# Kernel tuning notes

Hardware: AMD Instinct MI355X
Metric: run time of the kernel (lower is better)

## Reference

```python
import jax, jax.numpy as jnp
import numpy as np

T, HID, H, KV, D = 2048, 2048, 16, 8, 128
EPS = 1e-6
THETA = 10000.0


def setup_inputs() -> dict:
    key = jax.random.key(0)
    ks = jax.random.split(key, 4)
    return {
        "positions": jnp.arange(T, dtype=jnp.int32),
        "hidden_states": jax.random.normal(ks[0], (T, HID), dtype=jnp.float32),
        "layernorm_weight": jnp.ones((HID,), dtype=jnp.float32),
        "qkv_weight": jax.random.normal(ks[1], ((H + 2 * KV) * D, HID), dtype=jnp.float32) * 0.02,
        "q_norm_weight": jnp.ones((D,), dtype=jnp.float32),
        "k_norm_weight": jnp.ones((D,), dtype=jnp.float32),
        "o_weight": jax.random.normal(ks[2], (HID, H * D), dtype=jnp.float32) * 0.02,
    }


def _rms(x, w, eps=EPS):
    var = jnp.mean(jnp.square(x), axis=-1, keepdims=True)
    return x * jax.lax.rsqrt(var + eps) * w


def _rope(x, pos):
    # NeoX-style rotary over full head_dim. x: [T, nH, D]
    inv_freq = 1.0 / (THETA ** (jnp.arange(0, D, 2, dtype=jnp.float32) / D))
    ang = pos.astype(jnp.float32)[:, None] * inv_freq  # [T, D/2]
    cos, sin = jnp.cos(ang)[:, None, :], jnp.sin(ang)[:, None, :]
    x1, x2 = x[..., : D // 2], x[..., D // 2 :]
    return jnp.concatenate([x1 * cos - x2 * sin, x2 * cos + x1 * sin], axis=-1)


def reference(positions, hidden_states, layernorm_weight, qkv_weight,
              q_norm_weight, k_norm_weight, o_weight):
    # Fused RMSNorm + QKV projection
    normed = _rms(hidden_states, layernorm_weight)                 # [T, HID]
    qkv = normed @ qkv_weight.T                                    # [T, (H+2KV)*D]
    q, k, v = jnp.split(qkv, [H * D, (H + KV) * D], axis=-1)
    q = _rms(q.reshape(T, H, D), q_norm_weight)                    # per-head q norm
    k = _rms(k.reshape(T, KV, D), k_norm_weight)                   # per-head k norm
    v = v.reshape(T, KV, D)
    # RoPE
    q = _rope(q, positions)
    k = _rope(k, positions)
    # GQA causal attention
    scale = D ** -0.5
    kr = jnp.repeat(k, H // KV, axis=1)                            # [T, H, D]
    vr = jnp.repeat(v, H // KV, axis=1)
    scores = jnp.einsum("qhd,khd->hqk", q, kr) * scale             # [H, T, T]
    mask = jnp.tril(jnp.ones((T, T), dtype=bool))
    scores = jnp.where(mask[None], scores, jnp.finfo(scores.dtype).min)
    attn = jax.nn.softmax(scores, axis=-1)
    out = jnp.einsum("hqk,khd->qhd", attn, vr).reshape(T, H * D)
    return out @ o_weight.T                                        # [T, HID]
```

## Files before the change

### kernel.cpp

```cpp
#include <hip/hip_runtime.h>
#include <cstdint>
#include <cstddef>

typedef __bf16 bf16;
typedef __attribute__((ext_vector_type(8))) __bf16 bf16x8;
typedef __attribute__((ext_vector_type(4))) __bf16 bf16x4v;
typedef __attribute__((ext_vector_type(4))) float f32x4;
typedef __attribute__((ext_vector_type(4))) short short4v;

#define T_N   2048
#define HID_N 2048
#define NH    16
#define NKV   8
#define HD    128

#define MFMA(a, b, c) __builtin_amdgcn_mfma_f32_16x16x32_bf16((a), (b), (c), 0, 0, 0)

__device__ __forceinline__ f32x4 MFMA16(short4v a, short4v b, f32x4 c) {
#if __has_builtin(__builtin_amdgcn_mfma_f32_16x16x16bf16_1k)
    return __builtin_amdgcn_mfma_f32_16x16x16bf16_1k(a, b, c, 0, 0, 0);
#else
    asm volatile("v_mfma_f32_16x16x16_bf16 %0, %1, %2, %0\n\ts_nop 7\n\ts_nop 7"
                 : "+v"(c) : "v"(a), "v"(b));
    return c;
#endif
}

__device__ __forceinline__ void gl_lds16(const void* g, void* l) {
    __builtin_amdgcn_global_load_lds(
        (const __attribute__((address_space(1))) unsigned int*)g,
        (__attribute__((address_space(3))) unsigned int*)l,
        16, 0, 0);
}

__device__ __forceinline__ uint32_t pk2(float a, float b) {
    union { bf16 h; unsigned short u; } ca, cb;
    ca.h = (bf16)a; cb.h = (bf16)b;
    return ((uint32_t)cb.u << 16) | ca.u;
}

__device__ __forceinline__ void y2cq(int y, int& ci, int& qt) {
    if (y < 25)       { ci = 0; qt = y + 7; }
    else if (y < 42)  { ci = 1; qt = y - 10; }
    else if (y < 51)  { ci = 2; qt = y - 19; }
    else if (y == 51) { ci = 3; qt = 31; }
    else { int z = y - 52; int k = 7 - (z >> 2); ci = z & 3; qt = 8 * ci + k - 1; }
}
__device__ __forceinline__ int yof(int ci, int qt) {
    int k = qt + 1 - 8 * ci;
    if (k >= 8) {
        if (ci == 0) return qt - 7;
        if (ci == 1) return qt + 10;
        if (ci == 2) return qt + 19;
        return 51;
    }
    return 52 + (7 - k) * 4 + ci;
}

__global__ __launch_bounds__(256) void k_f2b(const float* __restrict__ in,
                                             bf16* __restrict__ out, int n) {
    int i = (blockIdx.x * 256 + threadIdx.x) * 8;
    if (i >= n) return;
    const float4* p = (const float4*)(in + i);
    float4 a = p[0], b = p[1];
    bf16x8 v;
    v[0] = (bf16)a.x; v[1] = (bf16)a.y; v[2] = (bf16)a.z; v[3] = (bf16)a.w;
    v[4] = (bf16)b.x; v[5] = (bf16)b.y; v[6] = (bf16)b.z; v[7] = (bf16)b.w;
    *(bf16x8*)(out + i) = v;
}

__global__ __launch_bounds__(256) void k_rmsnorm(const float* __restrict__ x,
                                                 const float* __restrict__ w,
                                                 bf16* __restrict__ out) {
    int row = blockIdx.x, tid = threadIdx.x;
    const float* xr = x + (size_t)row * HID_N;
    float4 a = ((const float4*)xr)[tid * 2];
    float4 b = ((const float4*)xr)[tid * 2 + 1];
    float ss = a.x*a.x + a.y*a.y + a.z*a.z + a.w*a.w
             + b.x*b.x + b.y*b.y + b.z*b.z + b.w*b.w;
    #pragma unroll
    for (int m = 32; m; m >>= 1) ss += __shfl_xor(ss, m);
    __shared__ float red[4];
    if ((tid & 63) == 0) red[tid >> 6] = ss;
    __syncthreads();
    float tot = red[0] + red[1] + red[2] + red[3];
    float rs = rsqrtf(tot * (1.0f / HID_N) + 1e-6f);
    const float4* wr = (const float4*)(w + tid * 8);
    float4 wa = wr[0], wb = wr[1];
    bf16x8 v;
    v[0] = (bf16)(a.x * rs * wa.x); v[1] = (bf16)(a.y * rs * wa.y);
    v[2] = (bf16)(a.z * rs * wa.z); v[3] = (bf16)(a.w * rs * wa.w);
    v[4] = (bf16)(b.x * rs * wb.x); v[5] = (bf16)(b.y * rs * wb.y);
    v[6] = (bf16)(b.z * rs * wb.z); v[7] = (bf16)(b.w * rs * wb.w);
    *(bf16x8*)(out + (size_t)row * HID_N + tid * 8) = v;
}

__global__ __launch_bounds__(256, 3) void k_gemm_bt(const bf16* __restrict__ A,
                                                    const bf16* __restrict__ B,
                                                    float* __restrict__ C,
                                                    int M, int N, int K) {
    __shared__ __attribute__((aligned(16))) bf16 As[128 * 64];
    __shared__ __attribute__((aligned(16))) bf16 Bs[128 * 64];
    const int tid = threadIdx.x;
    const int lane = tid & 63, wid = tid >> 6;
    const int wm = wid >> 1, wn = wid & 1;
    const int r = lane & 15, g = lane >> 4;
    const size_t bm = (size_t)blockIdx.y * 128, bn = (size_t)blockIdx.x * 128;

    f32x4 acc[4][4] = {};

    const int srow = tid >> 3;
    const int schk = tid & 7;

    for (int k0 = 0; k0 < K; k0 += 64) {
        __syncthreads();
        #pragma unroll
        for (int c = 0; c < 4; c++) {
            int row = c * 32 + srow;
            int ka = (schk ^ (row & 7)) << 3;
            gl_lds16(A + (bm + row) * (size_t)K + k0 + ka,
                     (char*)As + c * 4096 + tid * 16);
            gl_lds16(B + (bn + row) * (size_t)K + k0 + ka,
                     (char*)Bs + c * 4096 + tid * 16);
        }
        __syncthreads();
        #pragma unroll
        for (int kk = 0; kk < 2; kk++) {
            bf16x8 af[4], bfr[4];
            #pragma unroll
            for (int m = 0; m < 4; m++) {
                int row = wm * 64 + m * 16 + r;
                af[m] = *(const bf16x8*)(As + row * 64 + (((kk * 4 + g) ^ (row & 7)) << 3));
            }
            #pragma unroll
            for (int n = 0; n < 4; n++) {
                int row = wn * 64 + n * 16 + r;
                bfr[n] = *(const bf16x8*)(Bs + row * 64 + (((kk * 4 + g) ^ (row & 7)) << 3));
            }
            #pragma unroll
            for (int m = 0; m < 4; m++)
                #pragma unroll
                for (int n = 0; n < 4; n++)
                    acc[m][n] = MFMA(af[m], bfr[n], acc[m][n]);
        }
    }
    #pragma unroll
    for (int m = 0; m < 4; m++)
        #pragma unroll
        for (int n = 0; n < 4; n++)
            #pragma unroll
            for (int j = 0; j < 4; j++) {
                size_t row = bm + wm * 64 + m * 16 + g * 4 + j;
                size_t col = bn + wn * 64 + n * 16 + r;
                C[row * (size_t)N + col] = acc[m][n][j];
            }
}

__global__ __launch_bounds__(256, 3) void k_gemm_qkv(const bf16* __restrict__ A,
                                                     const bf16* __restrict__ B,
                                                     bf16* __restrict__ qkv3,
                                                     bf16* __restrict__ vb) {
    const int K = HID_N;
    __shared__ __attribute__((aligned(16))) bf16 As[128 * 64];
    __shared__ __attribute__((aligned(16))) bf16 Bs[128 * 64];
    const int tid = threadIdx.x;
    const int lane = tid & 63, wid = tid >> 6;
    const int wm = wid >> 1, wn = wid & 1;
    const int r = lane & 15, g = lane >> 4;
    const size_t bm = (size_t)blockIdx.y * 128, bn = (size_t)blockIdx.x * 128;

    f32x4 acc[4][4] = {};
    const int srow = tid >> 3;
    const int schk = tid & 7;

    for (int k0 = 0; k0 < K; k0 += 64) {
        __syncthreads();
        #pragma unroll
        for (int c = 0; c < 4; c++) {
            int row = c * 32 + srow;
            int ka = (schk ^ (row & 7)) << 3;
            gl_lds16(A + (bm + row) * (size_t)K + k0 + ka,
                     (char*)As + c * 4096 + tid * 16);
            gl_lds16(B + (bn + row) * (size_t)K + k0 + ka,
                     (char*)Bs + c * 4096 + tid * 16);
        }
        __syncthreads();
        #pragma unroll
        for (int kk = 0; kk < 2; kk++) {
            bf16x8 af[4], bfr[4];
            #pragma unroll
            for (int m = 0; m < 4; m++) {
                int row = wm * 64 + m * 16 + r;
                af[m] = *(const bf16x8*)(As + row * 64 + (((kk * 4 + g) ^ (row & 7)) << 3));
            }
            #pragma unroll
            for (int n = 0; n < 4; n++) {
                int row = wn * 64 + n * 16 + r;
                bfr[n] = *(const bf16x8*)(Bs + row * 64 + (((kk * 4 + g) ^ (row & 7)) << 3));
            }
            #pragma unroll
            for (int m = 0; m < 4; m++)
                #pragma unroll
                for (int n = 0; n < 4; n++)
                    acc[m][n] = MFMA(af[m], bfr[n], acc[m][n]);
        }
    }
    #pragma unroll
    for (int m = 0; m < 4; m++)
        #pragma unroll
        for (int n = 0; n < 4; n++)
            #pragma unroll
            for (int j = 0; j < 4; j++) {
                size_t row = bm + wm * 64 + m * 16 + g * 4 + j;
                size_t col = bn + wn * 64 + n * 16 + r;
                bf16 val = (bf16)acc[m][n][j];
                if (col < 3072) qkv3[row * 3072 + col] = val;
                else            vb[row * 1024 + (col - 3072)] = val;
            }
}

__global__ __launch_bounds__(256) void k_vt(const bf16* __restrict__ in,
                                            bf16* __restrict__ outp) {
    __shared__ bf16 tile[64][72];
    const int tb = blockIdx.x;
    const int db = blockIdx.y;
    const int tid = threadIdx.x;
    const int row = tid >> 2, cc = tid & 3;
    const bf16* src = in + (size_t)(tb * 64 + row) * 1024 + db * 64 + cc * 16;
    bf16x8 a = *(const bf16x8*)(src);
    bf16x8 b = *(const bf16x8*)(src + 8);
    #pragma unroll
    for (int i = 0; i < 8; i++) tile[row][cc * 16 + i] = a[i];
    #pragma unroll
    for (int i = 0; i < 8; i++) tile[row][cc * 16 + 8 + i] = b[i];
    __syncthreads();
    bf16* dst = outp + (size_t)(db * 64 + row) * 2048 + tb * 64 + cc * 16;
    bf16x8 o1, o2;
    #pragma unroll
    for (int i = 0; i < 8; i++) o1[i] = tile[cc * 16 + i][row];
    #pragma unroll
    for (int i = 0; i < 8; i++) o2[i] = tile[cc * 16 + 8 + i][row];
    *(bf16x8*)dst = o1;
    *(bf16x8*)(dst + 8) = o2;
}

__global__ __launch_bounds__(256) void k_normrope(const bf16* __restrict__ qkv3,
                                                  const float* __restrict__ qw,
                                                  const float* __restrict__ kw,
                                                  const int* __restrict__ pos,
                                                  bf16* __restrict__ q,
                                                  bf16* __restrict__ k) {
    const int t = blockIdx.x, tid = threadIdx.x;
    const int half = tid >> 7, d = tid & 127;
    const int slot = blockIdx.y * 2 + half;
    const bool isq = slot < 16;
    const int h = isq ? slot : slot - 16;
    float x = (float)qkv3[(size_t)t * 3072 + slot * 128 + d];
    float ss = x * x;
    #pragma unroll
    for (int m = 32; m; m >>= 1) ss += __shfl_xor(ss, m);
    __shared__ float red[4];
    __shared__ float sh[256];
    if ((tid & 63) == 0) red[tid >> 6] = ss;
    __syncthreads();
    float rs = rsqrtf((red[half * 2] + red[half * 2 + 1]) * (1.0f / HD) + 1e-6f);
    float nx = x * rs * (isq ? qw[d] : kw[d]);
    sh[tid] = nx;
    __syncthreads();
    float other = sh[tid ^ 64];
    int j = d & 63;
    float ang = (float)pos[t] * __powf(10000.f, -(float)j * (1.f / 64.f));
    float s, c;
    __sincosf(ang, &s, &c);
    float o = (d < 64) ? (nx * c - other * s) : (nx * c + other * s);
    bf16* dst = isq ? (q + ((size_t)t * NH + h) * HD + d)
                    : (k + ((size_t)t * NKV + h) * HD + d);
    *dst = (bf16)o;
}

__global__ __launch_bounds__(256, 3) void k_flash(const bf16* __restrict__ Q,
                                                  const bf16* __restrict__ K,
                                                  const bf16* __restrict__ VT,
                                                  bf16* __restrict__ On,
                                                  float* __restrict__ ml) {
    __shared__ __attribute__((aligned(16))) bf16 Ks2[2][64 * 128];
    __shared__ __attribute__((aligned(16))) bf16 Vt[128 * 64];

    const int tid = threadIdx.x, lane = tid & 63, w = tid >> 6;
    const int r = lane & 15, g = lane >> 4;
    const int h = blockIdx.x, y = blockIdx.y;
    int ci, qt;
    y2cq(y, ci, qt);
    const int c0 = ci * 8;
    const int ntl = min(qt + 1 - c0, 8);
    const int q0 = qt * 64;
    const int gh = h >> 1;
    const int q0w = q0 + w * 16;

    const int rowk = tid >> 4, posc = tid & 15;
    const int vrow = tid >> 3, vkb = tid & 7;
    const bf16* VTh = VT + (size_t)gh * 128 * 2048;

    bf16x8 qf[4];
    #pragma unroll
    for (int ks = 0; ks < 4; ks++)
        qf[ks] = *(const bf16x8*)(Q + ((size_t)(q0w + r) * NH + h) * HD + ks * 32 + g * 8);

    f32x4 acc[8] = {};
    float m_run = -1e30f, l_run = 0.f;
    const float scale = 0.08838834764831845f;

    {
        const int kv0 = c0 * 64;
        #pragma unroll
        for (int c = 0; c < 4; c++) {
            int row = c * 16 + rowk;
            int srcc = posc ^ (row & 7);
            gl_lds16(K + ((size_t)(kv0 + row) * NKV + gh) * HD + srcc * 8,
                     (char*)&Ks2[0][0] + c * 4096 + tid * 16);
        }
        asm volatile("s_waitcnt vmcnt(0)" ::: "memory");
        __builtin_amdgcn_s_barrier();
    }

    for (int t = 0; t < ntl; ++t) {
        const int b = t & 1;
        const int kv0 = (c0 + t) * 64;
        const bool pf = (t + 1 < ntl);
        #pragma unroll
        for (int it = 0; it < 4; it++) {
            int d = it * 32 + vrow;
            int srck = (vkb ^ (vrow & 7)) * 8;
            gl_lds16(VTh + (size_t)d * 2048 + kv0 + srck,
                     (char*)&Vt[0] + it * 4096 + tid * 16);
        }
        if (pf) {
            const int kv1 = kv0 + 64;
            #pragma unroll
            for (int c = 0; c < 4; c++) {
                int row = c * 16 + rowk;
                int srcc = posc ^ (row & 7);
                gl_lds16(K + ((size_t)(kv1 + row) * NKV + gh) * HD + srcc * 8,
                         (char*)&Ks2[0][0] + (b ^ 1) * 16384 + c * 4096 + tid * 16);
            }
        }
        const bool compute = (kv0 <= q0w + 15);
        union PB { uint32_t u[2]; short4v s; };
        PB pbu[4];
        if (compute) {
            const bf16* Kb = &Ks2[b][0];
            const bool fullt = (kv0 + 63 <= q0w);
            float sc[4][4];
            __builtin_amdgcn_s_setprio(1);
            #pragma unroll
            for (int t4 = 0; t4 < 4; t4++) {
                f32x4 S = {};
                #pragma unroll
                for (int ks = 0; ks < 4; ks++) {
                    int row = t4 * 16 + r;
                    bf16x8 kf = *(const bf16x8*)(Kb + row * 128 + (((4 * ks + g) ^ (row & 7)) * 8));
                    S = MFMA(kf, qf[ks], S);
                }
                if (fullt) {
                    #pragma unroll
                    for (int j = 0; j < 4; j++) sc[t4][j] = S[j] * scale;
                } else {
                    #pragma unroll
                    for (int j = 0; j < 4; j++) {
                        int kg = kv0 + t4 * 16 + 4 * g + j;
                        sc[t4][j] = (kg <= q0w + r) ? S[j] * scale : -1e30f;
                    }
                }
            }
            __builtin_amdgcn_s_setprio(0);
            float mx = sc[0][0];
            #pragma unroll
            for (int t4 = 0; t4 < 4; t4++)
                #pragma unroll
                for (int j = 0; j < 4; j++) mx = fmaxf(mx, sc[t4][j]);
            mx = fmaxf(mx, __shfl_xor(mx, 16));
            mx = fmaxf(mx, __shfl_xor(mx, 32));
            const bool nr = __all(mx <= m_run + 8.0f) != 0;
            float mn, alpha;
            if (nr) { mn = m_run; alpha = 1.0f; }
            else    { mn = fmaxf(m_run, mx); alpha = __expf(m_run - mn); m_run = mn; }
            float rsum = 0.f;
            #pragma unroll
            for (int t4 = 0; t4 < 4; t4++)
                #pragma unroll
                for (int j = 0; j < 4; j++) {
                    sc[t4][j] = __expf(sc[t4][j] - mn);
                    rsum += sc[t4][j];
                }
            rsum += __shfl_xor(rsum, 16);
            rsum += __shfl_xor(rsum, 32);
            l_run = l_run * alpha + rsum;
            if (!nr) {
                #pragma unroll
                for (int f = 0; f < 8; f++)
                    #pragma unroll
                    for (int j = 0; j < 4; j++) acc[f][j] *= alpha;
            }
            #pragma unroll
            for (int t4 = 0; t4 < 4; t4++) {
                pbu[t4].u[0] = pk2(sc[t4][0], sc[t4][1]);
                pbu[t4].u[1] = pk2(sc[t4][2], sc[t4][3]);
            }
        }
        if (pf) asm volatile("s_waitcnt vmcnt(4)" ::: "memory");
        else    asm volatile("s_waitcnt vmcnt(0)" ::: "memory");
        __builtin_amdgcn_s_barrier();
        if (compute) {
            const char* Vb = (const char*)&Vt[0];
            __builtin_amdgcn_s_setprio(1);
            #pragma unroll
            for (int f = 0; f < 8; f++) {
                #pragma unroll
                for (int t4 = 0; t4 < 4; t4++) {
                    short4v vf = *(const short4v*)(Vb + f * 2048 + r * 128 +
                                  (((2 * t4 + (g >> 1)) ^ (r & 7)) * 16) + (g & 1) * 8);
                    acc[f] = MFMA16(vf, pbu[t4].s, acc[f]);
                }
            }
            __builtin_amdgcn_s_setprio(0);
        }
        asm volatile("s_waitcnt vmcnt(0)" ::: "memory");
        __builtin_amdgcn_s_barrier();
    }
    const int lr = w * 16 + r;
    float inv_l = 1.0f / l_run;
    bf16* Ob = On + ((size_t)(h * 80 + y)) * 8192 + lr * 128;
    #pragma unroll
    for (int f = 0; f < 8; f++) {
        bf16x4v ov;
        #pragma unroll
        for (int j = 0; j < 4; j++) ov[j] = (bf16)(acc[f][j] * inv_l);
        *(bf16x4v*)(Ob + f * 16 + 4 * g) = ov;
    }
    if (g == 0) {
        float* mlp = ml + ((size_t)(h * 80 + y)) * 128;
        mlp[lr] = m_run;
        mlp[64 + lr] = l_run;
    }
}

__global__ __launch_bounds__(256) void k_comb(const bf16* __restrict__ On,
                                              const float* __restrict__ ml,
                                              bf16* __restrict__ ao) {
    const int h = blockIdx.x, qt = blockIdx.y;
    const int tid = threadIdx.x;
    const int dc = tid & 15;
    const int qr = tid >> 4;
    const int nc = 1 + (qt >= 8) + (qt >= 16) + (qt >= 24);
    int ys[4];
    #pragma unroll
    for (int i = 0; i < 4; i++) ys[i] = (i < nc) ? yof(i, qt) : 0;
    #pragma unroll
    for (int p = 0; p < 4; p++) {
        const int lq = p * 16 + qr;
        float mi[4], li[4], wi[4];
        float mstar = -1e30f;
        for (int i = 0; i < 4; i++) {
            if (i < nc) {
                const float* pml = ml + ((size_t)(h * 80 + ys[i])) * 128;
                mi[i] = pml[lq]; li[i] = pml[64 + lq];
                mstar = fmaxf(mstar, mi[i]);
            }
        }
        float wsum = 0.f;
        for (int i = 0; i < 4; i++) {
            if (i < nc) { wi[i] = li[i] * __expf(mi[i] - mstar); wsum += wi[i]; }
            else wi[i] = 0.f;
        }
        float inv = 1.f / wsum;
        float o[8] = {};
        for (int i = 0; i < 4; i++) {
            if (i < nc) {
                bf16x8 v = *(const bf16x8*)(On + ((size_t)(h * 80 + ys[i])) * 8192 +
                                            lq * 128 + dc * 8);
                float wn = wi[i] * inv;
                #pragma unroll
                for (int j = 0; j < 8; j++) o[j] += wn * (float)v[j];
            }
        }
        bf16x8 ov;
        #pragma unroll
        for (int j = 0; j < 8; j++) ov[j] = (bf16)o[j];
        const int q = qt * 64 + lq;
        *(bf16x8*)(ao + ((size_t)q * NH + h) * HD + dc * 8) = ov;
    }
}

extern "C" void kernel_launch(void* const* d_in, const int* in_sizes, int n_in,
                              void* d_out, int out_size, void* d_ws, size_t ws_size,
                              hipStream_t stream) {
    const int*   pos  = (const int*)d_in[0];
    const float* hid  = (const float*)d_in[1];
    const float* lw   = (const float*)d_in[2];
    const float* qkvw = (const float*)d_in[3];
    const float* qnw  = (const float*)d_in[4];
    const float* knw  = (const float*)d_in[5];
    const float* ow   = (const float*)d_in[6];
    float* out = (float*)d_out;

    char* ws = (char*)d_ws;
    bf16*  qkvw_b = (bf16*)(ws);
    bf16*  ow_b   = (bf16*)(ws + (16u << 20));
    bf16*  normed = (bf16*)(ws + (24u << 20));
    bf16*  qkv3   = (bf16*)(ws + (32u << 20));
    bf16*  qb     = (bf16*)(ws + (64u << 20));
    bf16*  kb     = (bf16*)(ws + (72u << 20));
    bf16*  vb     = (bf16*)(ws + (76u << 20));
    bf16*  ao     = normed;
    bf16*  On     = (bf16*)(ws + (32u << 20));
    float* ml     = (float*)(ws + (54u << 20));
    bf16*  vT     = (bf16*)(ws + (56u << 20));

    k_f2b<<<4096, 256, 0, stream>>>(qkvw, qkvw_b, 4096 * 2048);
    k_f2b<<<2048, 256, 0, stream>>>(ow, ow_b, 2048 * 2048);
    k_rmsnorm<<<T_N, 256, 0, stream>>>(hid, lw, normed);
    k_gemm_qkv<<<dim3(32, 16), 256, 0, stream>>>(normed, qkvw_b, qkv3, vb);
    k_vt<<<dim3(32, 16), 256, 0, stream>>>(vb, vT);
    k_normrope<<<dim3(T_N, 12), 256, 0, stream>>>(qkv3, qnw, knw, pos, qb, kb);
    k_flash<<<dim3(NH, 80), 256, 0, stream>>>(qb, kb, vT, On, ml);
    k_comb<<<dim3(NH, 32), 256, 0, stream>>>(On, ml, ao);
    k_gemm_bt<<<dim3(16, 16), 256, 0, stream>>>(ao, ow_b, out, 2048, 2048, 2048);
}
```

Measured before the change: 181.9 us.

## Merge weight conversions, shrink output GEMM tile, remap workgroups across XCDs

The two fp32-to-bf16 weight conversion launches are merged into one kernel launch. The output projection GEMM moves from 128x128 tiles (256 blocks) to 64x128 tiles (512 blocks), so all compute units on the device get work. Both GEMMs now remap the linear block id so that consecutive tiles land on the same XCD, aiming for better L2 reuse. The smaller tile lowers arithmetic intensity per block, and the remap hardcodes the grid sizes.

```diff
diff --git a/kernel.cpp b/kernel.cpp
--- a/kernel.cpp
+++ b/kernel.cpp
@@ -57,16 +57,19 @@
     return 52 + (7 - k) * 4 + ci;
 }
 
-__global__ __launch_bounds__(256) void k_f2b(const float* __restrict__ in,
-                                             bf16* __restrict__ out, int n) {
+__global__ __launch_bounds__(256) void k_f2b2(const float* __restrict__ a,
+                                              bf16* __restrict__ oa, int na,
+                                              const float* __restrict__ b,
+                                              bf16* __restrict__ ob, int nb) {
     int i = (blockIdx.x * 256 + threadIdx.x) * 8;
-    if (i >= n) return;
-    const float4* p = (const float4*)(in + i);
-    float4 a = p[0], b = p[1];
+    const float* src; bf16* dst; int j;
+    if (i < na) { src = a + i; dst = oa + i; }
+    else { j = i - na; if (j >= nb) return; src = b + j; dst = ob + j; }
+    float4 x = ((const float4*)src)[0], y = ((const float4*)src)[1];
     bf16x8 v;
-    v[0] = (bf16)a.x; v[1] = (bf16)a.y; v[2] = (bf16)a.z; v[3] = (bf16)a.w;
-    v[4] = (bf16)b.x; v[5] = (bf16)b.y; v[6] = (bf16)b.z; v[7] = (bf16)b.w;
-    *(bf16x8*)(out + i) = v;
+    v[0] = (bf16)x.x; v[1] = (bf16)x.y; v[2] = (bf16)x.z; v[3] = (bf16)x.w;
+    v[4] = (bf16)y.x; v[5] = (bf16)y.y; v[6] = (bf16)y.z; v[7] = (bf16)y.w;
+    *(bf16x8*)dst = v;
 }
 
 __global__ __launch_bounds__(256) void k_rmsnorm(const float* __restrict__ x,
@@ -95,63 +98,68 @@
     *(bf16x8*)(out + (size_t)row * HID_N + tid * 8) = v;
 }
 
-__global__ __launch_bounds__(256, 3) void k_gemm_bt(const bf16* __restrict__ A,
-                                                    const bf16* __restrict__ B,
-                                                    float* __restrict__ C,
-                                                    int M, int N, int K) {
-    __shared__ __attribute__((aligned(16))) bf16 As[128 * 64];
+__global__ __launch_bounds__(256, 3) void k_gemm_bt64(const bf16* __restrict__ A,
+                                                      const bf16* __restrict__ B,
+                                                      float* __restrict__ C,
+                                                      int M, int N, int K) {
+    __shared__ __attribute__((aligned(16))) bf16 As[64 * 64];
     __shared__ __attribute__((aligned(16))) bf16 Bs[128 * 64];
     const int tid = threadIdx.x;
     const int lane = tid & 63, wid = tid >> 6;
-    const int wm = wid >> 1, wn = wid & 1;
     const int r = lane & 15, g = lane >> 4;
-    const size_t bm = (size_t)blockIdx.y * 128, bn = (size_t)blockIdx.x * 128;
-
-    f32x4 acc[4][4] = {};
-
+    const int orig = blockIdx.y * gridDim.x + blockIdx.x;
+    const int wgid = (orig & 7) * 64 + (orig >> 3);
+    const size_t bm = (size_t)(wgid >> 4) * 64, bn = (size_t)(wgid & 15) * 128;
+
+    f32x4 acc[4][2] = {};
     const int srow = tid >> 3;
     const int schk = tid & 7;
 
     for (int k0 = 0; k0 < K; k0 += 64) {
         __syncthreads();
         #pragma unroll
-        for (int c = 0; c < 4; c++) {
+        for (int c = 0; c < 2; c++) {
             int row = c * 32 + srow;
             int ka = (schk ^ (row & 7)) << 3;
             gl_lds16(A + (bm + row) * (size_t)K + k0 + ka,
                      (char*)As + c * 4096 + tid * 16);
+        }
+        #pragma unroll
+        for (int c = 0; c < 4; c++) {
+            int row = c * 32 + srow;
+            int ka = (schk ^ (row & 7)) << 3;
             gl_lds16(B + (bn + row) * (size_t)K + k0 + ka,
                      (char*)Bs + c * 4096 + tid * 16);
         }
         __syncthreads();
         #pragma unroll
         for (int kk = 0; kk < 2; kk++) {
-            bf16x8 af[4], bfr[4];
+            bf16x8 af[4], bfr[2];
             #pragma unroll
             for (int m = 0; m < 4; m++) {
-                int row = wm * 64 + m * 16 + r;
+                int row = m * 16 + r;
                 af[m] = *(const bf16x8*)(As + row * 64 + (((kk * 4 + g) ^ (row & 7)) << 3));
             }
             #pragma unroll
-            for (int n = 0; n < 4; n++) {
-                int row = wn * 64 + n * 16 + r;
+            for (int n = 0; n < 2; n++) {
+                int row = wid * 32 + n * 16 + r;
                 bfr[n] = *(const bf16x8*)(Bs + row * 64 + (((kk * 4 + g) ^ (row & 7)) << 3));
             }
             #pragma unroll
             for (int m = 0; m < 4; m++)
                 #pragma unroll
-                for (int n = 0; n < 4; n++)
+                for (int n = 0; n < 2; n++)
                     acc[m][n] = MFMA(af[m], bfr[n], acc[m][n]);
         }
     }
     #pragma unroll
     for (int m = 0; m < 4; m++)
         #pragma unroll
-        for (int n = 0; n < 4; n++)
+        for (int n = 0; n < 2; n++)
             #pragma unroll
             for (int j = 0; j < 4; j++) {
-                size_t row = bm + wm * 64 + m * 16 + g * 4 + j;
-                size_t col = bn + wn * 64 + n * 16 + r;
+                size_t row = bm + m * 16 + g * 4 + j;
+                size_t col = bn + wid * 32 + n * 16 + r;
                 C[row * (size_t)N + col] = acc[m][n][j];
             }
 }
@@ -167,7 +175,9 @@
     const int lane = tid & 63, wid = tid >> 6;
     const int wm = wid >> 1, wn = wid & 1;
     const int r = lane & 15, g = lane >> 4;
-    const size_t bm = (size_t)blockIdx.y * 128, bn = (size_t)blockIdx.x * 128;
+    const int orig = blockIdx.y * gridDim.x + blockIdx.x;
+    const int wgid = (orig & 7) * 64 + (orig >> 3);
+    const size_t bm = (size_t)(wgid >> 5) * 128, bn = (size_t)(wgid & 31) * 128;
 
     f32x4 acc[4][4] = {};
     const int srow = tid >> 3;
@@ -516,13 +526,12 @@
     float* ml     = (float*)(ws + (54u << 20));
     bf16*  vT     = (bf16*)(ws + (56u << 20));
 
-    k_f2b<<<4096, 256, 0, stream>>>(qkvw, qkvw_b, 4096 * 2048);
-    k_f2b<<<2048, 256, 0, stream>>>(ow, ow_b, 2048 * 2048);
+    k_f2b2<<<6144, 256, 0, stream>>>(qkvw, qkvw_b, 4096 * 2048, ow, ow_b, 2048 * 2048);
     k_rmsnorm<<<T_N, 256, 0, stream>>>(hid, lw, normed);
     k_gemm_qkv<<<dim3(32, 16), 256, 0, stream>>>(normed, qkvw_b, qkv3, vb);
     k_vt<<<dim3(32, 16), 256, 0, stream>>>(vb, vT);
     k_normrope<<<dim3(T_N, 12), 256, 0, stream>>>(qkv3, qnw, knw, pos, qb, kb);
     k_flash<<<dim3(NH, 80), 256, 0, stream>>>(qb, kb, vT, On, ml);
     k_comb<<<dim3(NH, 32), 256, 0, stream>>>(On, ml, ao);
-    k_gemm_bt<<<dim3(16, 16), 256, 0, stream>>>(ao, ow_b, out, 2048, 2048, 2048);
-}
+    k_gemm_bt64<<<dim3(16, 32), 256, 0, stream>>>(ao, ow_b, out, 2048, 2048, 2048);
+}
```

Measured after the change: 175.6 us. 3.4% less time.
